# Performance work log

Measured on AMD Instinct MI355X. Metric: run time of the kernel, lower is better.

## Reference

```python
import jax, jax.numpy as jnp
import numpy as np

B, S, V, E, H, T = 512, 512, 5000, 100, 128, 25
HD = H // 2          # per-direction LSTM hidden size
START, STOP = 1, 2   # tag_map['START'], tag_map['STOP']


def setup_inputs() -> dict:
    key = jax.random.key(0)
    ks = jax.random.split(key, 20)
    sc = 0.1
    transitions = jax.random.normal(ks[0], (T, T), dtype=jnp.float32)
    transitions = transitions.at[:, START].set(-1000.0)
    transitions = transitions.at[STOP, :].set(-1000.0)
    return {
        "sentences": jax.random.randint(ks[1], (B, S), 0, V),
        "tags": jax.random.randint(ks[2], (B, S), 0, T),
        "embed": jax.random.normal(ks[3], (V, E), dtype=jnp.float32) * sc,
        # torch nn.LSTM weights, gate order (i, f, g, o), forward + backward dirs
        "W_ih_f": jax.random.normal(ks[4], (4 * HD, E), dtype=jnp.float32) * sc,
        "W_hh_f": jax.random.normal(ks[5], (4 * HD, HD), dtype=jnp.float32) * sc,
        "b_ih_f": jax.random.normal(ks[6], (4 * HD,), dtype=jnp.float32) * sc,
        "b_hh_f": jax.random.normal(ks[7], (4 * HD,), dtype=jnp.float32) * sc,
        "W_ih_b": jax.random.normal(ks[8], (4 * HD, E), dtype=jnp.float32) * sc,
        "W_hh_b": jax.random.normal(ks[9], (4 * HD, HD), dtype=jnp.float32) * sc,
        "b_ih_b": jax.random.normal(ks[10], (4 * HD,), dtype=jnp.float32) * sc,
        "b_hh_b": jax.random.normal(ks[11], (4 * HD,), dtype=jnp.float32) * sc,
        # init_hidden() uses randn initial states; materialized here as inputs
        "h0": jax.random.normal(ks[12], (2, B, HD), dtype=jnp.float32),
        "c0": jax.random.normal(ks[13], (2, B, HD), dtype=jnp.float32),
        "W_out": jax.random.normal(ks[14], (T, H), dtype=jnp.float32) * sc,
        "b_out": jax.random.normal(ks[15], (T,), dtype=jnp.float32) * sc,
        "transitions": transitions,
    }


def _lstm_dir(x, Wih, Whh, bih, bhh, h0, c0, reverse):
    # x: [B, S, E] -> outputs [B, S, HD]; torch gate order i, f, g, o
    def step(carry, xt):
        h, c = carry
        z = xt @ Wih.T + h @ Whh.T + (bih + bhh)  # [B, 4*HD]
        i, f, g, o = jnp.split(z, 4, axis=-1)
        c = jax.nn.sigmoid(f) * c + jax.nn.sigmoid(i) * jnp.tanh(g)
        h = jax.nn.sigmoid(o) * jnp.tanh(c)
        return (h, c), h
    _, hs = jax.lax.scan(step, (h0, c0), jnp.swapaxes(x, 0, 1), reverse=reverse)
    return jnp.swapaxes(hs, 0, 1)


def reference(sentences, tags, embed, W_ih_f, W_hh_f, b_ih_f, b_hh_f,
              W_ih_b, W_hh_b, b_ih_b, b_hh_b, h0, c0, W_out, b_out, transitions):
    # ---- BiLSTM features (eval mode: single-layer LSTM, dropout inactive) ----
    emb = embed[sentences]  # [B, S, E]
    hf = _lstm_dir(emb, W_ih_f, W_hh_f, b_ih_f, b_hh_f, h0[0], c0[0], False)
    hb = _lstm_dir(emb, W_ih_b, W_hh_b, b_ih_b, b_hh_b, h0[1], c0[1], True)
    logits = jnp.concatenate([hf, hb], axis=-1) @ W_out.T + b_out  # [B, S, T]

    # ---- real_path_score (gold path), batched ----
    lab = jnp.concatenate(
        [jnp.full((B, 1), START, dtype=tags.dtype), tags], axis=1)  # [B, S+1]
    em = jnp.take_along_axis(logits, lab[:, 1:, None], axis=2)[..., 0].sum(-1)
    tr = transitions[lab[:, :-1], lab[:, 1:]].sum(-1) + transitions[lab[:, -1], STOP]
    real = em + tr  # [B]

    # ---- total_score: CRF forward algorithm (previous starts at zeros, as in source) ----
    def fstep(prev, lt):  # prev [B, T], lt [B, T]
        # scores[b, i, j] = prev[b, i] + trans[i, j] + lt[b, j]
        sc = prev[:, :, None] + transitions[None, :, :] + lt[:, None, :]
        return jax.nn.logsumexp(sc, axis=1), None
    prev, _ = jax.lax.scan(fstep, jnp.zeros((B, T), logits.dtype),
                           jnp.swapaxes(logits, 0, 1))
    total = jax.nn.logsumexp(prev + transitions[:, STOP][None, :], axis=1)  # [B]

    # neg_log_likelihood sums over the batch
    return jnp.sum(total - real)
```

## Files before the change

kernel.cpp:

```cpp
#include <hip/hip_runtime.h>
#include <hip/hip_bf16.h>
#include <cstdint>

#define B_ 512
#define S_ 512
#define V_ 5000
#define E_ 100
#define HD_ 64
#define T_ 25
#define START_ 1
#define STOP_ 2

typedef _Float16 half2_t __attribute__((ext_vector_type(2)));
typedef __attribute__((ext_vector_type(8))) short short8;
typedef __attribute__((ext_vector_type(4))) float f32x4;

#if __has_builtin(__builtin_amdgcn_fdot2)
__device__ inline float dot2(uint32_t a, uint32_t b, float c) {
  return __builtin_amdgcn_fdot2(__builtin_bit_cast(half2_t, a),
                                __builtin_bit_cast(half2_t, b), c, false);
}
#else
__device__ inline float dot2(uint32_t a, uint32_t b, float c) {
  half2_t ha = __builtin_bit_cast(half2_t, a);
  half2_t hb = __builtin_bit_cast(half2_t, b);
  return c + (float)ha[0] * (float)hb[0] + (float)ha[1] * (float)hb[1];
}
#endif

__device__ inline float sigm(float x) { return 1.0f / (1.0f + __expf(-x)); }
__device__ inline float tanh_(float x) { return 1.0f - 2.0f / (1.0f + __expf(2.0f * x)); }

__global__ __launch_bounds__(256) void k_proj(const float* __restrict__ embed,
                                              const float* __restrict__ Wf,
                                              const float* __restrict__ Wb,
                                              float* __restrict__ Pf,
                                              float* __restrict__ Pb) {
  __shared__ __align__(16) float embS[16 * E_];
  int v0 = blockIdx.x * 16;
  const float* Wih = blockIdx.y ? Wb : Wf;
  float* P = blockIdx.y ? Pb : Pf;
  int nv = V_ - v0; if (nv > 16) nv = 16;
  for (int idx = threadIdx.x; idx < nv * E_; idx += 256)
    embS[idx] = embed[v0 * E_ + idx];
  __syncthreads();
  int u = threadIdx.x;
  float acc[16];
#pragma unroll
  for (int i = 0; i < 16; i++) acc[i] = 0.f;
  const float4* W4 = (const float4*)(Wih + u * E_);
  const float4* e4 = (const float4*)embS;
#pragma unroll 5
  for (int q = 0; q < 25; q++) {
    float4 w = W4[q];
#pragma unroll
    for (int vi = 0; vi < 16; vi++) {
      float4 e = e4[vi * 25 + q];
      acc[vi] += w.x * e.x + w.y * e.y + w.z * e.z + w.w * e.w;
    }
  }
  int pk = (u & 63) * 4 + (u >> 6);
  for (int vi = 0; vi < nv; vi++)
    P[(size_t)(v0 + vi) * 256 + pk] = acc[vi];
}

__global__ __launch_bounds__(256) void k_prep(const float* __restrict__ Wout,
                                              __hip_bfloat16* __restrict__ WoutP) {
  int idx = blockIdx.x * 256 + threadIdx.x;
  if (idx < 32 * 128) {
    int r = idx >> 7, c = idx & 127;
    float v = (r < T_) ? Wout[r * 128 + c] : 0.f;
    WoutP[idx] = __float2bfloat16(v);
  }
}

__global__ __launch_bounds__(64, 1) void k_lstm(
    const int* __restrict__ sentences,
    const float* __restrict__ Pf, const float* __restrict__ Pb,
    const float* __restrict__ Whh_f, const float* __restrict__ Whh_b,
    const float* __restrict__ bih_f, const float* __restrict__ bhh_f,
    const float* __restrict__ bih_b, const float* __restrict__ bhh_b,
    const float* __restrict__ h0, const float* __restrict__ c0,
    __hip_bfloat16* __restrict__ feat) {
  int j = threadIdx.x;
  int seq = blockIdx.x;
  int be = seq & (B_ - 1);
  int d = seq >> 9;
  const float* P   = d ? Pb : Pf;
  const float* Whh = d ? Whh_b : Whh_f;
  const float* bih = d ? bih_b : bih_f;
  const float* bhh = d ? bhh_b : bhh_f;

  __shared__ __align__(16) uint32_t hS[32];

  uint32_t wp[4][32];
  float bg[4];
#pragma unroll
  for (int g = 0; g < 4; g++) {
    int u = g * 64 + j;
    const float4* rp = (const float4*)(Whh + (size_t)u * HD_);
#pragma unroll
    for (int q = 0; q < 16; q++) {
      float4 a = rp[q];
      union { _Float16 h[2]; uint32_t u32; } p0, p1;
      p0.h[0] = (_Float16)a.x; p0.h[1] = (_Float16)a.y;
      p1.h[0] = (_Float16)a.z; p1.h[1] = (_Float16)a.w;
      wp[g][2 * q] = p0.u32; wp[g][2 * q + 1] = p1.u32;
    }
    bg[g] = bih[u] + bhh[u];
  }
  float c = c0[(d * B_ + be) * HD_ + j];
  ((_Float16*)hS)[j] = (_Float16)h0[(d * B_ + be) * HD_ + j];
  asm volatile("s_waitcnt lgkmcnt(0)" ::: "memory");

  const int* sent = sentences + (size_t)be * S_;
  int tt0 = d ? (S_ - 1) : 0;
  int stp = d ? -1 : 1;
  int tok1 = sent[tt0];
  const float4* P4 = (const float4*)P;
  float4 x = P4[(size_t)tok1 * 64 + j];
  tok1 = (S_ > 1) ? sent[tt0 + stp] : tok1;
  const uint4* hS4 = (const uint4*)hS;

  for (int t = 0; t < S_; t++) {
    int tt = tt0 + stp * t;
    float4 xn = x;
    if (t + 1 < S_) xn = P4[(size_t)tok1 * 64 + j];
    int tok2 = tok1;
    if (t + 2 < S_) tok2 = sent[tt + 2 * stp];

    float a0 = 0.f, a1 = 0.f, a2 = 0.f, a3 = 0.f;
    float b0 = 0.f, b1 = 0.f, b2 = 0.f, b3 = 0.f;
#pragma unroll
    for (int q = 0; q < 8; q++) {
      uint4 hv = hS4[q];
      int kp = 4 * q;
      a0 = dot2(wp[0][kp], hv.x, a0); b0 = dot2(wp[0][kp + 1], hv.y, b0);
      a0 = dot2(wp[0][kp + 2], hv.z, a0); b0 = dot2(wp[0][kp + 3], hv.w, b0);
      a1 = dot2(wp[1][kp], hv.x, a1); b1 = dot2(wp[1][kp + 1], hv.y, b1);
      a1 = dot2(wp[1][kp + 2], hv.z, a1); b1 = dot2(wp[1][kp + 3], hv.w, b1);
      a2 = dot2(wp[2][kp], hv.x, a2); b2 = dot2(wp[2][kp + 1], hv.y, b2);
      a2 = dot2(wp[2][kp + 2], hv.z, a2); b2 = dot2(wp[2][kp + 3], hv.w, b2);
      a3 = dot2(wp[3][kp], hv.x, a3); b3 = dot2(wp[3][kp + 1], hv.y, b3);
      a3 = dot2(wp[3][kp + 2], hv.z, a3); b3 = dot2(wp[3][kp + 3], hv.w, b3);
    }
    float zi = a0 + b0 + bg[0] + x.x;
    float zf = a1 + b1 + bg[1] + x.y;
    float zg = a2 + b2 + bg[2] + x.z;
    float zo = a3 + b3 + bg[3] + x.w;
    c = sigm(zf) * c + sigm(zi) * tanh_(zg);
    float hh = sigm(zo) * tanh_(c);
    feat[((size_t)be * S_ + tt) * 128 + d * 64 + j] = __float2bfloat16(hh);
    ((_Float16*)hS)[j] = (_Float16)hh;
    asm volatile("s_waitcnt lgkmcnt(0)" ::: "memory");
    x = xn;
    tok1 = tok2;
  }
}

__global__ __launch_bounds__(256) void k_logits(const __hip_bfloat16* __restrict__ feat,
                                                const __hip_bfloat16* __restrict__ WoutP,
                                                const float* __restrict__ bout,
                                                float* __restrict__ logits) {
  int w = threadIdx.x >> 6, l = threadIdx.x & 63;
  size_t r0 = ((size_t)blockIdx.x * 4 + w) * 16;
  int mrow = l & 15, kg = l >> 4;
  short8 bfr[2][4];
#pragma unroll
  for (int nt = 0; nt < 2; nt++) {
    int n = nt * 16 + mrow;
#pragma unroll
    for (int kb = 0; kb < 4; kb++)
      bfr[nt][kb] = *(const short8*)(WoutP + n * 128 + kb * 32 + kg * 8);
  }
  f32x4 acc[2];
#pragma unroll
  for (int nt = 0; nt < 2; nt++) {
    int col = nt * 16 + mrow;
    float bb = (col < T_) ? bout[col] : 0.f;
    acc[nt] = (f32x4){bb, bb, bb, bb};
  }
#pragma unroll
  for (int kb = 0; kb < 4; kb++) {
    short8 a = *(const short8*)(feat + (r0 + mrow) * 128 + kb * 32 + kg * 8);
    acc[0] = __builtin_amdgcn_mfma_f32_16x16x32_bf16(a, bfr[0][kb], acc[0], 0, 0, 0);
    acc[1] = __builtin_amdgcn_mfma_f32_16x16x32_bf16(a, bfr[1][kb], acc[1], 0, 0, 0);
  }
#pragma unroll
  for (int nt = 0; nt < 2; nt++) {
    int col = nt * 16 + mrow;
    if (col < T_) {
#pragma unroll
      for (int q = 0; q < 4; q++) {
        int row = kg * 4 + q;
        logits[(r0 + row) * T_ + col] = acc[nt][q];
      }
    }
  }
}

__global__ __launch_bounds__(64) void k_crf(const float* __restrict__ logits,
                                            const float* __restrict__ trans,
                                            float* __restrict__ totals) {
  int j = threadIdx.x;
  int b = blockIdx.x;
  bool act = j < T_;
  __shared__ __align__(16) float qS[32];
  float Ecol[T_];
#pragma unroll
  for (int i = 0; i < T_; i++)
    Ecol[i] = act ? __expf(trans[i * T_ + j]) : 0.f;
  if (j >= T_ && j < 32) qS[j] = 0.f;
  float tstop = act ? trans[j * T_ + STOP_] : 0.f;
  float prev = act ? 0.f : -INFINITY;
  const float* lg = logits + (size_t)b * S_ * T_;
  float ltn = act ? lg[j] : 0.f;
  asm volatile("s_waitcnt lgkmcnt(0)" ::: "memory");
  for (int t = 0; t < S_; t++) {
    float lt = ltn;
    if (t + 1 < S_) ltn = act ? lg[(size_t)(t + 1) * T_ + j] : 0.f;
    float m = __builtin_bit_cast(float,
        __builtin_amdgcn_readfirstlane(__builtin_bit_cast(int, prev)));
    float q = __expf(prev - m);
    if (act) qS[j] = q;
    asm volatile("s_waitcnt lgkmcnt(0)" ::: "memory");
    const float4* q4 = (const float4*)qS;
    float4 qv0 = q4[0], qv1 = q4[1], qv2 = q4[2], qv3 = q4[3];
    float4 qv4 = q4[4], qv5 = q4[5], qv6 = q4[6];
    float s0, s1, s2, s3;
    s0 = qv0.x * Ecol[0];  s1 = qv0.y * Ecol[1];
    s2 = qv0.z * Ecol[2];  s3 = qv0.w * Ecol[3];
    s0 += qv1.x * Ecol[4];  s1 += qv1.y * Ecol[5];
    s2 += qv1.z * Ecol[6];  s3 += qv1.w * Ecol[7];
    s0 += qv2.x * Ecol[8];  s1 += qv2.y * Ecol[9];
    s2 += qv2.z * Ecol[10]; s3 += qv2.w * Ecol[11];
    s0 += qv3.x * Ecol[12]; s1 += qv3.y * Ecol[13];
    s2 += qv3.z * Ecol[14]; s3 += qv3.w * Ecol[15];
    s0 += qv4.x * Ecol[16]; s1 += qv4.y * Ecol[17];
    s2 += qv4.z * Ecol[18]; s3 += qv4.w * Ecol[19];
    s0 += qv5.x * Ecol[20]; s1 += qv5.y * Ecol[21];
    s2 += qv5.z * Ecol[22]; s3 += qv5.w * Ecol[23];
    s0 += qv6.x * Ecol[24];
    float s = (s0 + s1) + (s2 + s3);
    prev = lt + m + __logf(s);
    if (!act) prev = -INFINITY;
  }
  float v = prev + tstop;
  float m = v;
#pragma unroll
  for (int off = 32; off > 0; off >>= 1)
    m = fmaxf(m, __shfl_xor(m, off, 64));
  float e = __expf(v - m);
#pragma unroll
  for (int off = 32; off > 0; off >>= 1)
    e += __shfl_xor(e, off, 64);
  if (j == 0) totals[b] = m + __logf(e);
}

__global__ __launch_bounds__(256) void k_real(const float* __restrict__ logits,
                                              const int* __restrict__ tags,
                                              const float* __restrict__ trans,
                                              float* __restrict__ reals) {
  __shared__ float red[256];
  int b = blockIdx.x;
  float acc = 0.f;
  for (int s = threadIdx.x; s < S_; s += 256) {
    int tg = tags[(size_t)b * S_ + s];
    int pv = (s == 0) ? START_ : tags[(size_t)b * S_ + s - 1];
    acc += logits[((size_t)b * S_ + s) * T_ + tg] + trans[pv * T_ + tg];
  }
  red[threadIdx.x] = acc;
  __syncthreads();
  for (int off = 128; off > 0; off >>= 1) {
    if (threadIdx.x < off) red[threadIdx.x] += red[threadIdx.x + off];
    __syncthreads();
  }
  if (threadIdx.x == 0)
    reals[b] = red[0] + trans[tags[(size_t)b * S_ + S_ - 1] * T_ + STOP_];
}

__global__ __launch_bounds__(256) void k_final(const float* __restrict__ totals,
                                               const float* __restrict__ reals,
                                               float* __restrict__ out) {
  __shared__ float red[256];
  float acc = 0.f;
  for (int b = threadIdx.x; b < B_; b += 256) acc += totals[b] - reals[b];
  red[threadIdx.x] = acc;
  __syncthreads();
  for (int off = 128; off > 0; off >>= 1) {
    if (threadIdx.x < off) red[threadIdx.x] += red[threadIdx.x + off];
    __syncthreads();
  }
  if (threadIdx.x == 0) out[0] = red[0];
}

extern "C" void kernel_launch(void* const* d_in, const int* in_sizes, int n_in,
                              void* d_out, int out_size, void* d_ws, size_t ws_size,
                              hipStream_t stream) {
  const int*   sentences = (const int*)d_in[0];
  const int*   tags  = (const int*)d_in[1];
  const float* embed = (const float*)d_in[2];
  const float* Wih_f = (const float*)d_in[3];
  const float* Whh_f = (const float*)d_in[4];
  const float* bih_f = (const float*)d_in[5];
  const float* bhh_f = (const float*)d_in[6];
  const float* Wih_b = (const float*)d_in[7];
  const float* Whh_b = (const float*)d_in[8];
  const float* bih_b = (const float*)d_in[9];
  const float* bhh_b = (const float*)d_in[10];
  const float* h0    = (const float*)d_in[11];
  const float* c0    = (const float*)d_in[12];
  const float* Wout  = (const float*)d_in[13];
  const float* bout  = (const float*)d_in[14];
  const float* trans = (const float*)d_in[15];

  char* ws = (char*)d_ws;
  float* Pf = (float*)(ws);
  float* Pb = (float*)(ws + 5120000);
  __hip_bfloat16* feat = (__hip_bfloat16*)(ws + 10240000);
  float* logits = (float*)(ws + 10240000 + 67108864);
  __hip_bfloat16* WoutP = (__hip_bfloat16*)(ws + 10240000 + 67108864 + 26214400);
  float* totals = (float*)(ws + 10240000 + 67108864 + 26214400 + 8192);
  float* reals  = totals + B_;
  float* out    = (float*)d_out;

  k_proj<<<dim3(313, 2), 256, 0, stream>>>(embed, Wih_f, Wih_b, Pf, Pb);
  k_prep<<<16, 256, 0, stream>>>(Wout, WoutP);
  k_lstm<<<1024, 64, 0, stream>>>(sentences, Pf, Pb, Whh_f, Whh_b,
                                  bih_f, bhh_f, bih_b, bhh_b, h0, c0, feat);
  k_logits<<<4096, 256, 0, stream>>>(feat, WoutP, bout, logits);
  k_crf<<<512, 64, 0, stream>>>(logits, trans, totals);
  k_real<<<512, 256, 0, stream>>>(logits, tags, trans, reals);
  k_final<<<1, 256, 0, stream>>>(totals, reals, out);
}
```

Measured before the change: 546.1 us.

## Split LSTM gate computation across two wavefronts per sequence

Each LSTM sequence block now uses two wavefronts: wave 0 computes the i and f gates and wave 1 computes the g and o gates. Wave 1 passes its activations to wave 0 through shared memory, and wave 0 updates the cell state and hidden vector. The precomputed input projection layout is reordered so each wave reads a contiguous float2 per step. This halves the per-thread dot-product work and the register weights, which may allow higher occupancy. The cost is two block barriers per timestep on the serial critical path.

```diff
diff --git a/kernel.cpp b/kernel.cpp
--- a/kernel.cpp
+++ b/kernel.cpp
@@ -59,7 +59,7 @@
       acc[vi] += w.x * e.x + w.y * e.y + w.z * e.z + w.w * e.w;
     }
   }
-  int pk = (u & 63) * 4 + (u >> 6);
+  int pk = (u >> 7) * 128 + (u & 63) * 2 + ((u >> 6) & 1);
   for (int vi = 0; vi < nv; vi++)
     P[(size_t)(v0 + vi) * 256 + pk] = acc[vi];
 }
@@ -74,7 +74,7 @@
   }
 }
 
-__global__ __launch_bounds__(64, 1) void k_lstm(
+__global__ __launch_bounds__(128) void k_lstm(
     const int* __restrict__ sentences,
     const float* __restrict__ Pf, const float* __restrict__ Pb,
     const float* __restrict__ Whh_f, const float* __restrict__ Whh_b,
@@ -82,7 +82,9 @@
     const float* __restrict__ bih_b, const float* __restrict__ bhh_b,
     const float* __restrict__ h0, const float* __restrict__ c0,
     __hip_bfloat16* __restrict__ feat) {
-  int j = threadIdx.x;
+  int tid = threadIdx.x;
+  int j = tid & 63;
+  int w = tid >> 6;
   int seq = blockIdx.x;
   int be = seq & (B_ - 1);
   int d = seq >> 9;
@@ -92,67 +94,79 @@
   const float* bhh = d ? bhh_b : bhh_f;
 
   __shared__ __align__(16) uint32_t hS[32];
-
-  uint32_t wp[4][32];
-  float bg[4];
-#pragma unroll
-  for (int g = 0; g < 4; g++) {
-    int u = g * 64 + j;
-    const float4* rp = (const float4*)(Whh + (size_t)u * HD_);
+  __shared__ __align__(16) float2 zS[64];
+
+  int u0 = w * 128 + j;
+  int u1 = u0 + 64;
+  uint32_t wA[32], wB[32];
+  {
+    const float4* r0 = (const float4*)(Whh + (size_t)u0 * HD_);
+    const float4* r1 = (const float4*)(Whh + (size_t)u1 * HD_);
 #pragma unroll
     for (int q = 0; q < 16; q++) {
-      float4 a = rp[q];
-      union { _Float16 h[2]; uint32_t u32; } p0, p1;
+      float4 a = r0[q], b = r1[q];
+      union { _Float16 h[2]; uint32_t u32; } p0, p1, p2, p3;
       p0.h[0] = (_Float16)a.x; p0.h[1] = (_Float16)a.y;
       p1.h[0] = (_Float16)a.z; p1.h[1] = (_Float16)a.w;
-      wp[g][2 * q] = p0.u32; wp[g][2 * q + 1] = p1.u32;
-    }
-    bg[g] = bih[u] + bhh[u];
-  }
-  float c = c0[(d * B_ + be) * HD_ + j];
-  ((_Float16*)hS)[j] = (_Float16)h0[(d * B_ + be) * HD_ + j];
-  asm volatile("s_waitcnt lgkmcnt(0)" ::: "memory");
+      p2.h[0] = (_Float16)b.x; p2.h[1] = (_Float16)b.y;
+      p3.h[0] = (_Float16)b.z; p3.h[1] = (_Float16)b.w;
+      wA[2 * q] = p0.u32; wA[2 * q + 1] = p1.u32;
+      wB[2 * q] = p2.u32; wB[2 * q + 1] = p3.u32;
+    }
+  }
+  float bA = bih[u0] + bhh[u0];
+  float bB = bih[u1] + bhh[u1];
+  float c = 0.f;
+  if (w == 0) {
+    c = c0[(d * B_ + be) * HD_ + j];
+    ((_Float16*)hS)[j] = (_Float16)h0[(d * B_ + be) * HD_ + j];
+  }
+  __syncthreads();
 
   const int* sent = sentences + (size_t)be * S_;
   int tt0 = d ? (S_ - 1) : 0;
   int stp = d ? -1 : 1;
   int tok1 = sent[tt0];
-  const float4* P4 = (const float4*)P;
-  float4 x = P4[(size_t)tok1 * 64 + j];
-  tok1 = (S_ > 1) ? sent[tt0 + stp] : tok1;
+  float2 x = *(const float2*)(P + (size_t)tok1 * 256 + w * 128 + 2 * j);
+  tok1 = sent[tt0 + stp];
   const uint4* hS4 = (const uint4*)hS;
 
   for (int t = 0; t < S_; t++) {
     int tt = tt0 + stp * t;
-    float4 xn = x;
-    if (t + 1 < S_) xn = P4[(size_t)tok1 * 64 + j];
+    float2 xn = x;
+    if (t + 1 < S_)
+      xn = *(const float2*)(P + (size_t)tok1 * 256 + w * 128 + 2 * j);
     int tok2 = tok1;
     if (t + 2 < S_) tok2 = sent[tt + 2 * stp];
 
-    float a0 = 0.f, a1 = 0.f, a2 = 0.f, a3 = 0.f;
-    float b0 = 0.f, b1 = 0.f, b2 = 0.f, b3 = 0.f;
+    float a0 = 0.f, a1 = 0.f, b0 = 0.f, b1 = 0.f;
 #pragma unroll
     for (int q = 0; q < 8; q++) {
       uint4 hv = hS4[q];
       int kp = 4 * q;
-      a0 = dot2(wp[0][kp], hv.x, a0); b0 = dot2(wp[0][kp + 1], hv.y, b0);
-      a0 = dot2(wp[0][kp + 2], hv.z, a0); b0 = dot2(wp[0][kp + 3], hv.w, b0);
-      a1 = dot2(wp[1][kp], hv.x, a1); b1 = dot2(wp[1][kp + 1], hv.y, b1);
-      a1 = dot2(wp[1][kp + 2], hv.z, a1); b1 = dot2(wp[1][kp + 3], hv.w, b1);
-      a2 = dot2(wp[2][kp], hv.x, a2); b2 = dot2(wp[2][kp + 1], hv.y, b2);
-      a2 = dot2(wp[2][kp + 2], hv.z, a2); b2 = dot2(wp[2][kp + 3], hv.w, b2);
-      a3 = dot2(wp[3][kp], hv.x, a3); b3 = dot2(wp[3][kp + 1], hv.y, b3);
-      a3 = dot2(wp[3][kp + 2], hv.z, a3); b3 = dot2(wp[3][kp + 3], hv.w, b3);
-    }
-    float zi = a0 + b0 + bg[0] + x.x;
-    float zf = a1 + b1 + bg[1] + x.y;
-    float zg = a2 + b2 + bg[2] + x.z;
-    float zo = a3 + b3 + bg[3] + x.w;
-    c = sigm(zf) * c + sigm(zi) * tanh_(zg);
-    float hh = sigm(zo) * tanh_(c);
-    feat[((size_t)be * S_ + tt) * 128 + d * 64 + j] = __float2bfloat16(hh);
-    ((_Float16*)hS)[j] = (_Float16)hh;
-    asm volatile("s_waitcnt lgkmcnt(0)" ::: "memory");
+      a0 = dot2(wA[kp + 0], hv.x, a0); a1 = dot2(wA[kp + 1], hv.y, a1);
+      a0 = dot2(wA[kp + 2], hv.z, a0); a1 = dot2(wA[kp + 3], hv.w, a1);
+      b0 = dot2(wB[kp + 0], hv.x, b0); b1 = dot2(wB[kp + 1], hv.y, b1);
+      b0 = dot2(wB[kp + 2], hv.z, b0); b1 = dot2(wB[kp + 3], hv.w, b1);
+    }
+    float zA = a0 + a1 + bA + x.x;
+    float zB = b0 + b1 + bB + x.y;
+    float tA = 0.f, tB = 0.f;
+    if (w == 1) {
+      zS[j] = make_float2(tanh_(zA), sigm(zB));
+    } else {
+      tA = sigm(zA);
+      tB = sigm(zB);
+    }
+    __syncthreads();
+    if (w == 0) {
+      float2 go = zS[j];
+      c = tB * c + tA * go.x;
+      float hh = go.y * tanh_(c);
+      feat[((size_t)be * S_ + tt) * 128 + d * 64 + j] = __float2bfloat16(hh);
+      ((_Float16*)hS)[j] = (_Float16)hh;
+    }
+    __syncthreads();
     x = xn;
     tok1 = tok2;
   }
@@ -326,8 +340,8 @@
 
   k_proj<<<dim3(313, 2), 256, 0, stream>>>(embed, Wih_f, Wih_b, Pf, Pb);
   k_prep<<<16, 256, 0, stream>>>(Wout, WoutP);
-  k_lstm<<<1024, 64, 0, stream>>>(sentences, Pf, Pb, Whh_f, Whh_b,
-                                  bih_f, bhh_f, bih_b, bhh_b, h0, c0, feat);
+  k_lstm<<<1024, 128, 0, stream>>>(sentences, Pf, Pb, Whh_f, Whh_b,
+                                   bih_f, bhh_f, bih_b, bhh_b, h0, c0, feat);
   k_logits<<<4096, 256, 0, stream>>>(feat, WoutP, bout, logits);
   k_crf<<<512, 64, 0, stream>>>(logits, trans, totals);
   k_real<<<512, 256, 0, stream>>>(logits, tags, trans, reals);
```

After: 658.0 us. 20.5% more time.

## Fuse CRF and gold-path kernels, use fast rcp, drop LDS waitcnts

Applied to the files above, without the earlier changes.

Merges the CRF forward and real-path-score kernels into one launch, with four batch rows per 256-thread block for the CRF part and separate blocks for the gold-path reduction, so the two can run concurrently. Replaces divisions in sigmoid/tanh with the hardware reciprocal. Replaces explicit s_waitcnt lgkmcnt(0) after LDS writes with a compiler-only memory fence in the LSTM and CRF loops. This relies on in-wave LDS ordering and compiler-inserted waits for correctness, and the approximate reciprocal may slightly change accuracy.

```diff
diff --git a/kernel.cpp b/kernel.cpp
--- a/kernel.cpp
+++ b/kernel.cpp
@@ -28,8 +28,15 @@
 }
 #endif
 
-__device__ inline float sigm(float x) { return 1.0f / (1.0f + __expf(-x)); }
-__device__ inline float tanh_(float x) { return 1.0f - 2.0f / (1.0f + __expf(2.0f * x)); }
+#if __has_builtin(__builtin_amdgcn_rcpf)
+__device__ inline float fastrcp(float x) { return __builtin_amdgcn_rcpf(x); }
+#else
+__device__ inline float fastrcp(float x) { return 1.0f / x; }
+#endif
+__device__ inline float sigm(float x) { return fastrcp(1.0f + __expf(-x)); }
+__device__ inline float tanh_(float x) { return 1.0f - 2.0f * fastrcp(1.0f + __expf(2.0f * x)); }
+
+#define LDS_FENCE() asm volatile("" ::: "memory")
 
 __global__ __launch_bounds__(256) void k_proj(const float* __restrict__ embed,
                                               const float* __restrict__ Wf,
@@ -111,7 +118,7 @@
   }
   float c = c0[(d * B_ + be) * HD_ + j];
   ((_Float16*)hS)[j] = (_Float16)h0[(d * B_ + be) * HD_ + j];
-  asm volatile("s_waitcnt lgkmcnt(0)" ::: "memory");
+  LDS_FENCE();
 
   const int* sent = sentences + (size_t)be * S_;
   int tt0 = d ? (S_ - 1) : 0;
@@ -119,7 +126,7 @@
   int tok1 = sent[tt0];
   const float4* P4 = (const float4*)P;
   float4 x = P4[(size_t)tok1 * 64 + j];
-  tok1 = (S_ > 1) ? sent[tt0 + stp] : tok1;
+  tok1 = sent[tt0 + stp];
   const uint4* hS4 = (const uint4*)hS;
 
   for (int t = 0; t < S_; t++) {
@@ -152,7 +159,7 @@
     float hh = sigm(zo) * tanh_(c);
     feat[((size_t)be * S_ + tt) * 128 + d * 64 + j] = __float2bfloat16(hh);
     ((_Float16*)hS)[j] = (_Float16)hh;
-    asm volatile("s_waitcnt lgkmcnt(0)" ::: "memory");
+    LDS_FENCE();
     x = xn;
     tok1 = tok2;
   }
@@ -199,84 +206,85 @@
   }
 }
 
-__global__ __launch_bounds__(64) void k_crf(const float* __restrict__ logits,
-                                            const float* __restrict__ trans,
-                                            float* __restrict__ totals) {
-  int j = threadIdx.x;
-  int b = blockIdx.x;
-  bool act = j < T_;
-  __shared__ __align__(16) float qS[32];
-  float Ecol[T_];
-#pragma unroll
-  for (int i = 0; i < T_; i++)
-    Ecol[i] = act ? __expf(trans[i * T_ + j]) : 0.f;
-  if (j >= T_ && j < 32) qS[j] = 0.f;
-  float tstop = act ? trans[j * T_ + STOP_] : 0.f;
-  float prev = act ? 0.f : -INFINITY;
-  const float* lg = logits + (size_t)b * S_ * T_;
-  float ltn = act ? lg[j] : 0.f;
-  asm volatile("s_waitcnt lgkmcnt(0)" ::: "memory");
-  for (int t = 0; t < S_; t++) {
-    float lt = ltn;
-    if (t + 1 < S_) ltn = act ? lg[(size_t)(t + 1) * T_ + j] : 0.f;
-    float m = __builtin_bit_cast(float,
-        __builtin_amdgcn_readfirstlane(__builtin_bit_cast(int, prev)));
-    float q = __expf(prev - m);
-    if (act) qS[j] = q;
-    asm volatile("s_waitcnt lgkmcnt(0)" ::: "memory");
-    const float4* q4 = (const float4*)qS;
-    float4 qv0 = q4[0], qv1 = q4[1], qv2 = q4[2], qv3 = q4[3];
-    float4 qv4 = q4[4], qv5 = q4[5], qv6 = q4[6];
-    float s0, s1, s2, s3;
-    s0 = qv0.x * Ecol[0];  s1 = qv0.y * Ecol[1];
-    s2 = qv0.z * Ecol[2];  s3 = qv0.w * Ecol[3];
-    s0 += qv1.x * Ecol[4];  s1 += qv1.y * Ecol[5];
-    s2 += qv1.z * Ecol[6];  s3 += qv1.w * Ecol[7];
-    s0 += qv2.x * Ecol[8];  s1 += qv2.y * Ecol[9];
-    s2 += qv2.z * Ecol[10]; s3 += qv2.w * Ecol[11];
-    s0 += qv3.x * Ecol[12]; s1 += qv3.y * Ecol[13];
-    s2 += qv3.z * Ecol[14]; s3 += qv3.w * Ecol[15];
-    s0 += qv4.x * Ecol[16]; s1 += qv4.y * Ecol[17];
-    s2 += qv4.z * Ecol[18]; s3 += qv4.w * Ecol[19];
-    s0 += qv5.x * Ecol[20]; s1 += qv5.y * Ecol[21];
-    s2 += qv5.z * Ecol[22]; s3 += qv5.w * Ecol[23];
-    s0 += qv6.x * Ecol[24];
-    float s = (s0 + s1) + (s2 + s3);
-    prev = lt + m + __logf(s);
-    if (!act) prev = -INFINITY;
-  }
-  float v = prev + tstop;
-  float m = v;
-#pragma unroll
-  for (int off = 32; off > 0; off >>= 1)
-    m = fmaxf(m, __shfl_xor(m, off, 64));
-  float e = __expf(v - m);
-#pragma unroll
-  for (int off = 32; off > 0; off >>= 1)
-    e += __shfl_xor(e, off, 64);
-  if (j == 0) totals[b] = m + __logf(e);
-}
-
-__global__ __launch_bounds__(256) void k_real(const float* __restrict__ logits,
-                                              const int* __restrict__ tags,
-                                              const float* __restrict__ trans,
-                                              float* __restrict__ reals) {
+__global__ __launch_bounds__(256) void k_crfreal(const float* __restrict__ logits,
+                                                 const int* __restrict__ tags,
+                                                 const float* __restrict__ trans,
+                                                 float* __restrict__ totals,
+                                                 float* __restrict__ reals) {
+  __shared__ __align__(16) float qS[4][32];
   __shared__ float red[256];
-  int b = blockIdx.x;
-  float acc = 0.f;
-  for (int s = threadIdx.x; s < S_; s += 256) {
-    int tg = tags[(size_t)b * S_ + s];
-    int pv = (s == 0) ? START_ : tags[(size_t)b * S_ + s - 1];
-    acc += logits[((size_t)b * S_ + s) * T_ + tg] + trans[pv * T_ + tg];
-  }
-  red[threadIdx.x] = acc;
-  __syncthreads();
-  for (int off = 128; off > 0; off >>= 1) {
-    if (threadIdx.x < off) red[threadIdx.x] += red[threadIdx.x + off];
+  int blk = blockIdx.x;
+  if (blk < 128) {
+    int w = threadIdx.x >> 6;
+    int j = threadIdx.x & 63;
+    int b = blk * 4 + w;
+    bool act = j < T_;
+    float Ecol[T_];
+#pragma unroll
+    for (int i = 0; i < T_; i++)
+      Ecol[i] = act ? __expf(trans[i * T_ + j]) : 0.f;
+    if (j >= T_ && j < 32) qS[w][j] = 0.f;
+    float tstop = act ? trans[j * T_ + STOP_] : 0.f;
+    float prev = act ? 0.f : -INFINITY;
+    const float* lg = logits + (size_t)b * S_ * T_;
+    float ltn = act ? lg[j] : 0.f;
+    LDS_FENCE();
+    for (int t = 0; t < S_; t++) {
+      float lt = ltn;
+      if (t + 1 < S_) ltn = act ? lg[(size_t)(t + 1) * T_ + j] : 0.f;
+      float m = __builtin_bit_cast(float,
+          __builtin_amdgcn_readfirstlane(__builtin_bit_cast(int, prev)));
+      float q = __expf(prev - m);
+      if (act) qS[w][j] = q;
+      LDS_FENCE();
+      const float4* q4 = (const float4*)qS[w];
+      float4 qv0 = q4[0], qv1 = q4[1], qv2 = q4[2], qv3 = q4[3];
+      float4 qv4 = q4[4], qv5 = q4[5], qv6 = q4[6];
+      float s0, s1, s2, s3;
+      s0 = qv0.x * Ecol[0];  s1 = qv0.y * Ecol[1];
+      s2 = qv0.z * Ecol[2];  s3 = qv0.w * Ecol[3];
+      s0 += qv1.x * Ecol[4];  s1 += qv1.y * Ecol[5];
+      s2 += qv1.z * Ecol[6];  s3 += qv1.w * Ecol[7];
+      s0 += qv2.x * Ecol[8];  s1 += qv2.y * Ecol[9];
+      s2 += qv2.z * Ecol[10]; s3 += qv2.w * Ecol[11];
+      s0 += qv3.x * Ecol[12]; s1 += qv3.y * Ecol[13];
+      s2 += qv3.z * Ecol[14]; s3 += qv3.w * Ecol[15];
+      s0 += qv4.x * Ecol[16]; s1 += qv4.y * Ecol[17];
+      s2 += qv4.z * Ecol[18]; s3 += qv4.w * Ecol[19];
+      s0 += qv5.x * Ecol[20]; s1 += qv5.y * Ecol[21];
+      s2 += qv5.z * Ecol[22]; s3 += qv5.w * Ecol[23];
+      s0 += qv6.x * Ecol[24];
+      float s = (s0 + s1) + (s2 + s3);
+      prev = lt + m + __logf(s);
+      if (!act) prev = -INFINITY;
+    }
+    float v = prev + tstop;
+    float m = v;
+#pragma unroll
+    for (int off = 32; off > 0; off >>= 1)
+      m = fmaxf(m, __shfl_xor(m, off, 64));
+    float e = __expf(v - m);
+#pragma unroll
+    for (int off = 32; off > 0; off >>= 1)
+      e += __shfl_xor(e, off, 64);
+    if (j == 0) totals[b] = m + __logf(e);
+  } else {
+    int b = blk - 128;
+    float acc = 0.f;
+    for (int s = threadIdx.x; s < S_; s += 256) {
+      int tg = tags[(size_t)b * S_ + s];
+      int pv = (s == 0) ? START_ : tags[(size_t)b * S_ + s - 1];
+      acc += logits[((size_t)b * S_ + s) * T_ + tg] + trans[pv * T_ + tg];
+    }
+    red[threadIdx.x] = acc;
     __syncthreads();
-  }
-  if (threadIdx.x == 0)
-    reals[b] = red[0] + trans[tags[(size_t)b * S_ + S_ - 1] * T_ + STOP_];
+    for (int off = 128; off > 0; off >>= 1) {
+      if (threadIdx.x < off) red[threadIdx.x] += red[threadIdx.x + off];
+      __syncthreads();
+    }
+    if (threadIdx.x == 0)
+      reals[b] = red[0] + trans[tags[(size_t)b * S_ + S_ - 1] * T_ + STOP_];
+  }
 }
 
 __global__ __launch_bounds__(256) void k_final(const float* __restrict__ totals,
@@ -329,7 +337,6 @@
   k_lstm<<<1024, 64, 0, stream>>>(sentences, Pf, Pb, Whh_f, Whh_b,
                                   bih_f, bhh_f, bih_b, bhh_b, h0, c0, feat);
   k_logits<<<4096, 256, 0, stream>>>(feat, WoutP, bout, logits);
-  k_crf<<<512, 64, 0, stream>>>(logits, trans, totals);
-  k_real<<<512, 256, 0, stream>>>(logits, tags, trans, reals);
+  k_crfreal<<<640, 256, 0, stream>>>(logits, tags, trans, totals, reals);
   k_final<<<1, 256, 0, stream>>>(totals, reals, out);
 }
```

After: 658.1 us. +20.5%, slower.

## Split CRF reduction across wave halves and double rows per logits wave

Applied to the files above, without the earlier changes.

The CRF forward kernel now divides the 25-term sum over previous tags between the two 32-lane halves of the wave, each half handling 13 terms, and combines the partial sums with a cross-half shuffle. This shortens the serial FMA chain in each time step. The logits kernel computes 32 rows per wave instead of 16, reusing the register-held W_out fragments across two M tiles, and launches half as many blocks. The CRF split adds a shuffle to every step and moves from vector to scalar LDS reads.

```diff
diff --git a/kernel.cpp b/kernel.cpp
--- a/kernel.cpp
+++ b/kernel.cpp
@@ -119,7 +119,7 @@
   int tok1 = sent[tt0];
   const float4* P4 = (const float4*)P;
   float4 x = P4[(size_t)tok1 * 64 + j];
-  tok1 = (S_ > 1) ? sent[tt0 + stp] : tok1;
+  tok1 = sent[tt0 + stp];
   const uint4* hS4 = (const uint4*)hS;
 
   for (int t = 0; t < S_; t++) {
@@ -163,7 +163,7 @@
                                                 const float* __restrict__ bout,
                                                 float* __restrict__ logits) {
   int w = threadIdx.x >> 6, l = threadIdx.x & 63;
-  size_t r0 = ((size_t)blockIdx.x * 4 + w) * 16;
+  size_t r0 = ((size_t)blockIdx.x * 4 + w) * 32;
   int mrow = l & 15, kg = l >> 4;
   short8 bfr[2][4];
 #pragma unroll
@@ -173,27 +173,38 @@
     for (int kb = 0; kb < 4; kb++)
       bfr[nt][kb] = *(const short8*)(WoutP + n * 128 + kb * 32 + kg * 8);
   }
-  f32x4 acc[2];
+  f32x4 acc[2][2];
+  float bb[2];
 #pragma unroll
   for (int nt = 0; nt < 2; nt++) {
     int col = nt * 16 + mrow;
-    float bb = (col < T_) ? bout[col] : 0.f;
-    acc[nt] = (f32x4){bb, bb, bb, bb};
-  }
+    bb[nt] = (col < T_) ? bout[col] : 0.f;
+  }
+#pragma unroll
+  for (int mt = 0; mt < 2; mt++)
+#pragma unroll
+    for (int nt = 0; nt < 2; nt++)
+      acc[mt][nt] = (f32x4){bb[nt], bb[nt], bb[nt], bb[nt]};
 #pragma unroll
   for (int kb = 0; kb < 4; kb++) {
-    short8 a = *(const short8*)(feat + (r0 + mrow) * 128 + kb * 32 + kg * 8);
-    acc[0] = __builtin_amdgcn_mfma_f32_16x16x32_bf16(a, bfr[0][kb], acc[0], 0, 0, 0);
-    acc[1] = __builtin_amdgcn_mfma_f32_16x16x32_bf16(a, bfr[1][kb], acc[1], 0, 0, 0);
-  }
-#pragma unroll
-  for (int nt = 0; nt < 2; nt++) {
-    int col = nt * 16 + mrow;
-    if (col < T_) {
-#pragma unroll
-      for (int q = 0; q < 4; q++) {
-        int row = kg * 4 + q;
-        logits[(r0 + row) * T_ + col] = acc[nt][q];
+    short8 am0 = *(const short8*)(feat + (r0 + mrow) * 128 + kb * 32 + kg * 8);
+    short8 am1 = *(const short8*)(feat + (r0 + 16 + mrow) * 128 + kb * 32 + kg * 8);
+    acc[0][0] = __builtin_amdgcn_mfma_f32_16x16x32_bf16(am0, bfr[0][kb], acc[0][0], 0, 0, 0);
+    acc[0][1] = __builtin_amdgcn_mfma_f32_16x16x32_bf16(am0, bfr[1][kb], acc[0][1], 0, 0, 0);
+    acc[1][0] = __builtin_amdgcn_mfma_f32_16x16x32_bf16(am1, bfr[0][kb], acc[1][0], 0, 0, 0);
+    acc[1][1] = __builtin_amdgcn_mfma_f32_16x16x32_bf16(am1, bfr[1][kb], acc[1][1], 0, 0, 0);
+  }
+#pragma unroll
+  for (int mt = 0; mt < 2; mt++) {
+#pragma unroll
+    for (int nt = 0; nt < 2; nt++) {
+      int col = nt * 16 + mrow;
+      if (col < T_) {
+#pragma unroll
+        for (int q = 0; q < 4; q++) {
+          int row = mt * 16 + kg * 4 + q;
+          logits[(r0 + row) * T_ + col] = acc[mt][nt][q];
+        }
       }
     }
   }
@@ -204,44 +215,47 @@
                                             float* __restrict__ totals) {
   int j = threadIdx.x;
   int b = blockIdx.x;
-  bool act = j < T_;
+  int half = j >> 5;
+  int jj = j & 31;
+  bool act = (half == 0) && (jj < T_);
+  bool pact = (jj < T_);
+  int bo = half ? 13 : 0;
+  float Evec[13];
+#pragma unroll
+  for (int k = 0; k < 13; k++) {
+    int i = bo + k;
+    Evec[k] = (pact && i < T_) ? __expf(trans[i * T_ + jj]) : 0.f;
+  }
   __shared__ __align__(16) float qS[32];
-  float Ecol[T_];
-#pragma unroll
-  for (int i = 0; i < T_; i++)
-    Ecol[i] = act ? __expf(trans[i * T_ + j]) : 0.f;
   if (j >= T_ && j < 32) qS[j] = 0.f;
-  float tstop = act ? trans[j * T_ + STOP_] : 0.f;
+  float tstop = act ? trans[jj * T_ + STOP_] : 0.f;
   float prev = act ? 0.f : -INFINITY;
   const float* lg = logits + (size_t)b * S_ * T_;
-  float ltn = act ? lg[j] : 0.f;
+  float ltn = act ? lg[jj] : 0.f;
   asm volatile("s_waitcnt lgkmcnt(0)" ::: "memory");
   for (int t = 0; t < S_; t++) {
     float lt = ltn;
-    if (t + 1 < S_) ltn = act ? lg[(size_t)(t + 1) * T_ + j] : 0.f;
+    if (t + 1 < S_) ltn = act ? lg[(size_t)(t + 1) * T_ + jj] : 0.f;
     float m = __builtin_bit_cast(float,
         __builtin_amdgcn_readfirstlane(__builtin_bit_cast(int, prev)));
     float q = __expf(prev - m);
     if (act) qS[j] = q;
     asm volatile("s_waitcnt lgkmcnt(0)" ::: "memory");
-    const float4* q4 = (const float4*)qS;
-    float4 qv0 = q4[0], qv1 = q4[1], qv2 = q4[2], qv3 = q4[3];
-    float4 qv4 = q4[4], qv5 = q4[5], qv6 = q4[6];
-    float s0, s1, s2, s3;
-    s0 = qv0.x * Ecol[0];  s1 = qv0.y * Ecol[1];
-    s2 = qv0.z * Ecol[2];  s3 = qv0.w * Ecol[3];
-    s0 += qv1.x * Ecol[4];  s1 += qv1.y * Ecol[5];
-    s2 += qv1.z * Ecol[6];  s3 += qv1.w * Ecol[7];
-    s0 += qv2.x * Ecol[8];  s1 += qv2.y * Ecol[9];
-    s2 += qv2.z * Ecol[10]; s3 += qv2.w * Ecol[11];
-    s0 += qv3.x * Ecol[12]; s1 += qv3.y * Ecol[13];
-    s2 += qv3.z * Ecol[14]; s3 += qv3.w * Ecol[15];
-    s0 += qv4.x * Ecol[16]; s1 += qv4.y * Ecol[17];
-    s2 += qv4.z * Ecol[18]; s3 += qv4.w * Ecol[19];
-    s0 += qv5.x * Ecol[20]; s1 += qv5.y * Ecol[21];
-    s2 += qv5.z * Ecol[22]; s3 += qv5.w * Ecol[23];
-    s0 += qv6.x * Ecol[24];
-    float s = (s0 + s1) + (s2 + s3);
+    float s0 = qS[bo + 0] * Evec[0];
+    float s1 = qS[bo + 1] * Evec[1];
+    float s2 = qS[bo + 2] * Evec[2];
+    float s3 = qS[bo + 3] * Evec[3];
+    s0 += qS[bo + 4] * Evec[4];
+    s1 += qS[bo + 5] * Evec[5];
+    s2 += qS[bo + 6] * Evec[6];
+    s3 += qS[bo + 7] * Evec[7];
+    s0 += qS[bo + 8] * Evec[8];
+    s1 += qS[bo + 9] * Evec[9];
+    s2 += qS[bo + 10] * Evec[10];
+    s3 += qS[bo + 11] * Evec[11];
+    s0 += qS[bo + 12] * Evec[12];
+    float sp = (s0 + s1) + (s2 + s3);
+    float s = sp + __shfl_xor(sp, 32, 64);
     prev = lt + m + __logf(s);
     if (!act) prev = -INFINITY;
   }
@@ -328,7 +342,7 @@
   k_prep<<<16, 256, 0, stream>>>(Wout, WoutP);
   k_lstm<<<1024, 64, 0, stream>>>(sentences, Pf, Pb, Whh_f, Whh_b,
                                   bih_f, bhh_f, bih_b, bhh_b, h0, c0, feat);
-  k_logits<<<4096, 256, 0, stream>>>(feat, WoutP, bout, logits);
+  k_logits<<<2048, 256, 0, stream>>>(feat, WoutP, bout, logits);
   k_crf<<<512, 64, 0, stream>>>(logits, trans, totals);
   k_real<<<512, 256, 0, stream>>>(logits, tags, trans, reals);
   k_final<<<1, 256, 0, stream>>>(totals, reals, out);
```

After: 556.6 us. About the same (+1.9%).
